# Performance work log

Hardware: AMD Instinct MI355X
Metric: run time of the kernel (lower is better)

Reference implementation:

```python
import jax, jax.numpy as jnp
import numpy as np

OUT_H, OUT_W = 7, 7          # pooled output size
MAX_GRID = 4                 # static bound on adaptive sampling grid (ROI sizes <= 28 px)


def _axis_interp(pos, size, grid_mask):
    """torchvision bilinear rules along one axis.
    pos: sample coords, grid_mask: which adaptive-grid slots are active.
    Returns low/high indices and masked interpolation weights."""
    valid = (pos >= -1.0) & (pos <= size)          # outside -> contributes 0
    p = jnp.maximum(pos, 0.0)
    low = jnp.minimum(jnp.floor(p).astype(jnp.int32), size - 1)
    high = jnp.minimum(low + 1, size - 1)
    p = jnp.where(low >= size - 1, jnp.float32(size - 1), p)  # clamp at top edge
    frac = p - low.astype(p.dtype)
    m = (valid & grid_mask).astype(p.dtype)
    return low, high, (1.0 - frac) * m, frac * m


def _roi_align(features, rois):
    B, C, H, W = features.shape
    bidx = rois[:, 0].astype(jnp.int32)
    x1, y1, x2, y2 = rois[:, 1], rois[:, 2], rois[:, 3], rois[:, 4]
    # spatial_scale = 1.0, aligned=False -> min ROI size of 1
    roi_w = jnp.maximum(x2 - x1, 1.0)
    roi_h = jnp.maximum(y2 - y1, 1.0)
    bin_h = roi_h / OUT_H
    bin_w = roi_w / OUT_W
    # sampling_ratio = -1 -> adaptive grid = ceil(roi_size / pooled_size)
    gh = jnp.clip(jnp.ceil(roi_h / OUT_H).astype(jnp.int32), 1, MAX_GRID)
    gw = jnp.clip(jnp.ceil(roi_w / OUT_W).astype(jnp.int32), 1, MAX_GRID)
    g = jnp.arange(MAX_GRID)
    py = jnp.arange(OUT_H)
    px = jnp.arange(OUT_W)
    # sample coords: [N, OUT, MAX_GRID]
    ys = (y1[:, None, None] + py[None, :, None] * bin_h[:, None, None]
          + (g[None, None, :] + 0.5) * bin_h[:, None, None] / gh[:, None, None].astype(jnp.float32))
    xs = (x1[:, None, None] + px[None, :, None] * bin_w[:, None, None]
          + (g[None, None, :] + 0.5) * bin_w[:, None, None] / gw[:, None, None].astype(jnp.float32))
    gm_y = g[None, None, :] < gh[:, None, None]
    gm_x = g[None, None, :] < gw[:, None, None]
    y_lo, y_hi, wy0, wy1 = _axis_interp(ys, H, gm_y)
    x_lo, x_hi, wx0, wx1 = _axis_interp(xs, W, gm_x)

    f = features.reshape(B, C, H * W)
    bb = bidx[:, None, None, None, None]
    acc = jnp.zeros((rois.shape[0], OUT_H, OUT_W, C), dtype=features.dtype)
    # 4 bilinear corners; gather [N,OH,Gy,OW,Gx,C] one corner at a time
    for yi, wy in ((y_lo, wy0), (y_hi, wy1)):
        for xi, wx in ((x_lo, wx0), (x_hi, wx1)):
            idx = yi[:, :, :, None, None] * W + xi[:, None, None, :, :]  # [N,OH,Gy,OW,Gx]
            vals = f[bb, :, idx]                                         # [N,OH,Gy,OW,Gx,C]
            w = wy[:, :, :, None, None] * wx[:, None, None, :, :]
            acc = acc + jnp.einsum('nygxhc,nygxh->nyxc', vals, w)
    count = jnp.maximum(gh * gw, 1).astype(features.dtype)
    out = acc / count[:, None, None, None]
    return jnp.transpose(out, (0, 3, 1, 2))  # [N, C, OUT_H, OUT_W]


def setup_inputs() -> dict:
    key = jax.random.key(0)
    kf, kb, kx, ky, kw, kh = jax.random.split(key, 6)
    B, C, H, W, N = 4, 256, 200, 272, 512
    features = jax.random.normal(kf, (B, C, H, W), dtype=jnp.float32)
    b = jax.random.randint(kb, (N,), 0, B).astype(jnp.float32)
    # box sizes in [7, 28] px so adaptive grid ceil(size/7) <= MAX_GRID=4
    bw = jax.random.uniform(kw, (N,), minval=7.0, maxval=28.0)
    bh = jax.random.uniform(kh, (N,), minval=7.0, maxval=28.0)
    x1 = jax.random.uniform(kx, (N,), minval=0.0, maxval=W - 29.0)
    y1 = jax.random.uniform(ky, (N,), minval=0.0, maxval=H - 29.0)
    rois = jnp.stack([b, x1, y1, x1 + bw, y1 + bh], axis=1)
    return {"features": features, "rois": rois}


def reference(features, rois):
    return _roi_align(features, rois)
```

## Files before the change

kernel.cpp:

```cpp
#include <hip/hip_runtime.h>

#define MAXG 4
#define CPB 8
#define UCOLS 33
#define PLANE 991
#define S2LEN (4 * PLANE)

__global__ __launch_bounds__(256, 5) void roi_align_kernel(
    const float* __restrict__ feat,
    const float* __restrict__ rois,
    float* __restrict__ out,
    int C, int H, int W)
{
    const int n    = blockIdx.x;
    const int cblk = blockIdx.y;
    const int t    = threadIdx.x;

    __shared__ float2 s_feat2[S2LEN];
    __shared__ int4   s_ypack[28];
    __shared__ int4   s_xpack[28];

    const float* roi = rois + (size_t)n * 5;
    const int   b  = (int)roi[0];
    const float x1 = roi[1], y1 = roi[2], x2 = roi[3], y2 = roi[4];
    const float roi_w = fmaxf(x2 - x1, 1.0f);
    const float roi_h = fmaxf(y2 - y1, 1.0f);
    const float bin_h = roi_h / 7.0f;
    const float bin_w = roi_w / 7.0f;
    int gh = (int)ceilf(roi_h / 7.0f); gh = min(max(gh, 1), MAXG);
    int gw = (int)ceilf(roi_w / 7.0f); gw = min(max(gw, 1), MAXG);
    const float inv_count = 1.0f / (float)(gh * gw);

    auto lo_of = [](float pos, int size) {
        float p = fmaxf(pos, 0.0f);
        return min((int)floorf(p), size - 1);
    };
    const int y0 = lo_of(y1 + 0.5f * bin_h / (float)gh, H);
    const int yE = min(lo_of(y1 + 6.0f * bin_h + ((float)(gh - 1) + 0.5f) * bin_h / (float)gh, H) + 1, H - 1);
    const int x0 = lo_of(x1 + 0.5f * bin_w / (float)gw, W);
    const int xE = min(lo_of(x1 + 6.0f * bin_w + ((float)(gw - 1) + 0.5f) * bin_w / (float)gw, W) + 1, W - 1);
    const int rh    = min(yE - y0 + 1, 30);
    const int x0a   = x0 & ~3;
    const int spanA = min(xE - x0a + 1, 33);
    const int CM    = W - 4 - x0a;

    if (t < 28) {
        const int py = t >> 2, g = t & 3;
        float pos  = y1 + (float)py * bin_h + ((float)g + 0.5f) * bin_h / (float)gh;
        bool valid = (pos >= -1.0f) && (pos <= (float)H);
        float p = fmaxf(pos, 0.0f);
        int lo  = min((int)floorf(p), H - 1);
        int hi  = min(lo + 1, H - 1);
        if (lo >= H - 1) p = (float)(H - 1);
        float frac = p - (float)lo;
        float m = valid ? 1.0f : 0.0f;
        s_ypack[t] = make_int4((lo - y0) * UCOLS, (hi - y0) * UCOLS,
                               __float_as_int((1.0f - frac) * m),
                               __float_as_int(frac * m));
    } else if (t < 56) {
        const int u = t - 28;
        const int px = u >> 2, g = u & 3;
        float pos  = x1 + (float)px * bin_w + ((float)g + 0.5f) * bin_w / (float)gw;
        bool valid = (pos >= -1.0f) && (pos <= (float)W);
        float p = fmaxf(pos, 0.0f);
        int lo  = min((int)floorf(p), W - 1);
        int hi  = min(lo + 1, W - 1);
        if (lo >= W - 1) p = (float)(W - 1);
        float frac = p - (float)lo;
        float m = valid ? 1.0f : 0.0f;
        s_xpack[u] = make_int4(lo - x0a, hi - x0a,
                               __float_as_int((1.0f - frac) * m),
                               __float_as_int(frac * m));
    }

    {
        const int  p    = t & 3;
        const int  q    = (t >> 2) & 7;
        const int  r0   = t >> 5;
        const int  q4   = q << 2;
        const bool qon  = (q4 < spanA);
        const int  colA = min(q4, CM);
        const bool tail = (q == 7) && (spanA == 33);

        const size_t HW = (size_t)H * W;
        const int c0 = cblk * CPB;
        const float* fbase = feat + ((size_t)b * C + c0) * HW + (size_t)y0 * W + x0a;
        const float* ga = fbase + (size_t)(2 * p) * HW;
        float2* sb = s_feat2 + p * PLANE;

        #pragma unroll
        for (int k = 0; k < 4; ++k) {
            const int r = r0 + (k << 3);
            if (r < rh) {
                const float* gp = ga + (size_t)r * W;
                if (qon) {
                    const float4 va = *(const float4*)(gp + colA);
                    const float4 vb = *(const float4*)(gp + HW + colA);
                    float2* sp = sb + r * UCOLS + colA;
                    sp[0] = make_float2(va.x, vb.x);
                    sp[1] = make_float2(va.y, vb.y);
                    sp[2] = make_float2(va.z, vb.z);
                    sp[3] = make_float2(va.w, vb.w);
                }
                if (tail) {
                    sb[r * UCOLS + 32] = make_float2(gp[32], gp[HW + 32]);
                }
            }
        }
    }
    __syncthreads();

    if (t < 196) {
        const int p   = t & 3;
        const int pix = t >> 2;
        const int py  = pix / 7;
        const int px  = pix - py * 7;
        const float2* sp = s_feat2 + p * PLANE;

        int4 xp[4];
        #pragma unroll
        for (int g = 0; g < 4; ++g) xp[g] = s_xpack[(px << 2) + g];

        float ax = 0.0f, ay = 0.0f;
        #pragma unroll
        for (int gy = 0; gy < MAXG; ++gy) {
            if (gy < gh) {
                const int4 yp = s_ypack[(py << 2) + gy];
                const float wy0 = __int_as_float(yp.z);
                const float wy1 = __int_as_float(yp.w);
                #pragma unroll
                for (int gx = 0; gx < MAXG; ++gx) {
                    if (gx < gw) {
                        const float wx0 = __int_as_float(xp[gx].z);
                        const float wx1 = __int_as_float(xp[gx].w);
                        const float2 v00 = sp[yp.x + xp[gx].x];
                        const float2 v01 = sp[yp.x + xp[gx].y];
                        const float2 v10 = sp[yp.y + xp[gx].x];
                        const float2 v11 = sp[yp.y + xp[gx].y];
                        ax += wy0 * (wx0 * v00.x + wx1 * v01.x)
                            + wy1 * (wx0 * v10.x + wx1 * v11.x);
                        ay += wy0 * (wx0 * v00.y + wx1 * v01.y)
                            + wy1 * (wx0 * v10.y + wx1 * v11.y);
                    }
                }
            }
        }
        const size_t ob = ((size_t)n * C + cblk * CPB + 2 * p) * 49 + pix;
        out[ob]      = ax * inv_count;
        out[ob + 49] = ay * inv_count;
    }
}

extern "C" void kernel_launch(void* const* d_in, const int* in_sizes, int n_in,
                              void* d_out, int out_size, void* d_ws, size_t ws_size,
                              hipStream_t stream) {
    const float* feat = (const float*)d_in[0];
    const float* rois = (const float*)d_in[1];
    float* out = (float*)d_out;

    const int C = 256, H = 200, W = 272;
    const int N = in_sizes[1] / 5;

    dim3 grid(N, C / CPB);
    roi_align_kernel<<<grid, 256, 0, stream>>>(feat, rois, out, C, H, W);
}
```

Before: 323.8 us.

## Process four ROIs per block with register-prefetched feature loads overlapping compute

Each block now handles four consecutive ROIs instead of one. While the current ROI's outputs are computed from shared memory, the next ROI's feature patch is loaded from global memory into registers, then written to shared memory after a barrier. The aim is to hide global load latency behind the interpolation math and to spread per-block launch overhead across more work. The cost is more registers (launch bounds lowered from 5 to 4 waves), extra barriers, and a grid that is four times smaller.

```diff
diff --git a/kernel.cpp b/kernel.cpp
--- a/kernel.cpp
+++ b/kernel.cpp
@@ -5,112 +5,134 @@
 #define UCOLS 33
 #define PLANE 991
 #define S2LEN (4 * PLANE)
-
-__global__ __launch_bounds__(256, 5) void roi_align_kernel(
-    const float* __restrict__ feat,
-    const float* __restrict__ rois,
-    float* __restrict__ out,
-    int C, int H, int W)
-{
-    const int n    = blockIdx.x;
-    const int cblk = blockIdx.y;
-    const int t    = threadIdx.x;
-
-    __shared__ float2 s_feat2[S2LEN];
-    __shared__ int4   s_ypack[28];
-    __shared__ int4   s_xpack[28];
-
+#define RPB 4
+
+
+struct RoiS {
+    float x1, y1, bin_h, bin_w;
+    int   gh, gw;
+    float inv_count;
+    int   y0, x0a, rh, spanA, CM;
+    const float* fbase;
+};
+
+__device__ __forceinline__ int lo_of(float pos, int size) {
+    float pp = fmaxf(pos, 0.0f);
+    return min((int)floorf(pp), size - 1);
+}
+
+__device__ __forceinline__ RoiS make_scalars(const float* __restrict__ rois, int n,
+                                             const float* __restrict__ feat,
+                                             int C, int c0, int H, int W, size_t HW) {
+    RoiS s;
     const float* roi = rois + (size_t)n * 5;
     const int   b  = (int)roi[0];
     const float x1 = roi[1], y1 = roi[2], x2 = roi[3], y2 = roi[4];
     const float roi_w = fmaxf(x2 - x1, 1.0f);
     const float roi_h = fmaxf(y2 - y1, 1.0f);
-    const float bin_h = roi_h / 7.0f;
-    const float bin_w = roi_w / 7.0f;
+    s.bin_h = roi_h / 7.0f;
+    s.bin_w = roi_w / 7.0f;
     int gh = (int)ceilf(roi_h / 7.0f); gh = min(max(gh, 1), MAXG);
     int gw = (int)ceilf(roi_w / 7.0f); gw = min(max(gw, 1), MAXG);
-    const float inv_count = 1.0f / (float)(gh * gw);
-
-    auto lo_of = [](float pos, int size) {
-        float p = fmaxf(pos, 0.0f);
-        return min((int)floorf(p), size - 1);
-    };
-    const int y0 = lo_of(y1 + 0.5f * bin_h / (float)gh, H);
-    const int yE = min(lo_of(y1 + 6.0f * bin_h + ((float)(gh - 1) + 0.5f) * bin_h / (float)gh, H) + 1, H - 1);
-    const int x0 = lo_of(x1 + 0.5f * bin_w / (float)gw, W);
-    const int xE = min(lo_of(x1 + 6.0f * bin_w + ((float)(gw - 1) + 0.5f) * bin_w / (float)gw, W) + 1, W - 1);
-    const int rh    = min(yE - y0 + 1, 30);
-    const int x0a   = x0 & ~3;
-    const int spanA = min(xE - x0a + 1, 33);
-    const int CM    = W - 4 - x0a;
-
+    s.gh = gh; s.gw = gw;
+    s.inv_count = 1.0f / (float)(gh * gw);
+    s.x1 = x1; s.y1 = y1;
+    s.y0 = lo_of(y1 + 0.5f * s.bin_h / (float)gh, H);
+    int yE = min(lo_of(y1 + 6.0f * s.bin_h + ((float)(gh - 1) + 0.5f) * s.bin_h / (float)gh, H) + 1, H - 1);
+    int x0 = lo_of(x1 + 0.5f * s.bin_w / (float)gw, W);
+    int xE = min(lo_of(x1 + 6.0f * s.bin_w + ((float)(gw - 1) + 0.5f) * s.bin_w / (float)gw, W) + 1, W - 1);
+    s.rh    = min(yE - s.y0 + 1, 30);
+    s.x0a   = x0 & ~3;
+    s.spanA = min(xE - s.x0a + 1, 33);
+    s.CM    = W - 4 - s.x0a;
+    s.fbase = feat + ((size_t)b * C + c0) * HW + (size_t)s.y0 * W + s.x0a;
+    return s;
+}
+
+__device__ __forceinline__ void issue_loads(const RoiS& s, int p, int q, int q4, int r0,
+                                            size_t HW, int W,
+                                            float4 va[4], float4 vb[4], float tc[4][2]) {
+    const bool qon  = (q4 < s.spanA);
+    const int  colA = min(q4, s.CM);
+    const bool tail = (q == 7) && (s.spanA == 33);
+    const float* ga = s.fbase + (size_t)(2 * p) * HW;
+    #pragma unroll
+    for (int k = 0; k < 4; ++k) {
+        const int r = r0 + (k << 3);
+        if (r < s.rh) {
+            const float* gp = ga + (size_t)r * W;
+            if (qon) {
+                va[k] = *(const float4*)(gp + colA);
+                vb[k] = *(const float4*)(gp + HW + colA);
+            }
+            if (tail) { tc[k][0] = gp[32]; tc[k][1] = gp[HW + 32]; }
+        }
+    }
+}
+
+__device__ __forceinline__ void write_lds(const RoiS& s, int p, int q, int q4, int r0,
+                                          float2* __restrict__ s_feat2,
+                                          const float4 va[4], const float4 vb[4],
+                                          const float tc[4][2]) {
+    const bool qon  = (q4 < s.spanA);
+    const int  colA = min(q4, s.CM);
+    const bool tail = (q == 7) && (s.spanA == 33);
+    float2* sb = s_feat2 + p * PLANE;
+    #pragma unroll
+    for (int k = 0; k < 4; ++k) {
+        const int r = r0 + (k << 3);
+        if (r < s.rh) {
+            if (qon) {
+                float2* sp = sb + r * UCOLS + colA;
+                sp[0] = make_float2(va[k].x, vb[k].x);
+                sp[1] = make_float2(va[k].y, vb[k].y);
+                sp[2] = make_float2(va[k].z, vb[k].z);
+                sp[3] = make_float2(va[k].w, vb[k].w);
+            }
+            if (tail) sb[r * UCOLS + 32] = make_float2(tc[k][0], tc[k][1]);
+        }
+    }
+}
+
+__device__ __forceinline__ void write_tables(const RoiS& s, int t, int H, int W,
+                                             int4* __restrict__ s_ypack,
+                                             int4* __restrict__ s_xpack) {
     if (t < 28) {
         const int py = t >> 2, g = t & 3;
-        float pos  = y1 + (float)py * bin_h + ((float)g + 0.5f) * bin_h / (float)gh;
+        float pos  = s.y1 + (float)py * s.bin_h + ((float)g + 0.5f) * s.bin_h / (float)s.gh;
         bool valid = (pos >= -1.0f) && (pos <= (float)H);
-        float p = fmaxf(pos, 0.0f);
-        int lo  = min((int)floorf(p), H - 1);
+        float pp = fmaxf(pos, 0.0f);
+        int lo  = min((int)floorf(pp), H - 1);
         int hi  = min(lo + 1, H - 1);
-        if (lo >= H - 1) p = (float)(H - 1);
-        float frac = p - (float)lo;
+        if (lo >= H - 1) pp = (float)(H - 1);
+        float frac = pp - (float)lo;
         float m = valid ? 1.0f : 0.0f;
-        s_ypack[t] = make_int4((lo - y0) * UCOLS, (hi - y0) * UCOLS,
+        s_ypack[t] = make_int4((lo - s.y0) * UCOLS, (hi - s.y0) * UCOLS,
                                __float_as_int((1.0f - frac) * m),
                                __float_as_int(frac * m));
     } else if (t < 56) {
         const int u = t - 28;
         const int px = u >> 2, g = u & 3;
-        float pos  = x1 + (float)px * bin_w + ((float)g + 0.5f) * bin_w / (float)gw;
+        float pos  = s.x1 + (float)px * s.bin_w + ((float)g + 0.5f) * s.bin_w / (float)s.gw;
         bool valid = (pos >= -1.0f) && (pos <= (float)W);
-        float p = fmaxf(pos, 0.0f);
-        int lo  = min((int)floorf(p), W - 1);
+        float pp = fmaxf(pos, 0.0f);
+        int lo  = min((int)floorf(pp), W - 1);
         int hi  = min(lo + 1, W - 1);
-        if (lo >= W - 1) p = (float)(W - 1);
-        float frac = p - (float)lo;
+        if (lo >= W - 1) pp = (float)(W - 1);
+        float frac = pp - (float)lo;
         float m = valid ? 1.0f : 0.0f;
-        s_xpack[u] = make_int4(lo - x0a, hi - x0a,
+        s_xpack[u] = make_int4(lo - s.x0a, hi - s.x0a,
                                __float_as_int((1.0f - frac) * m),
                                __float_as_int(frac * m));
     }
-
-    {
-        const int  p    = t & 3;
-        const int  q    = (t >> 2) & 7;
-        const int  r0   = t >> 5;
-        const int  q4   = q << 2;
-        const bool qon  = (q4 < spanA);
-        const int  colA = min(q4, CM);
-        const bool tail = (q == 7) && (spanA == 33);
-
-        const size_t HW = (size_t)H * W;
-        const int c0 = cblk * CPB;
-        const float* fbase = feat + ((size_t)b * C + c0) * HW + (size_t)y0 * W + x0a;
-        const float* ga = fbase + (size_t)(2 * p) * HW;
-        float2* sb = s_feat2 + p * PLANE;
-
-        #pragma unroll
-        for (int k = 0; k < 4; ++k) {
-            const int r = r0 + (k << 3);
-            if (r < rh) {
-                const float* gp = ga + (size_t)r * W;
-                if (qon) {
-                    const float4 va = *(const float4*)(gp + colA);
-                    const float4 vb = *(const float4*)(gp + HW + colA);
-                    float2* sp = sb + r * UCOLS + colA;
-                    sp[0] = make_float2(va.x, vb.x);
-                    sp[1] = make_float2(va.y, vb.y);
-                    sp[2] = make_float2(va.z, vb.z);
-                    sp[3] = make_float2(va.w, vb.w);
-                }
-                if (tail) {
-                    sb[r * UCOLS + 32] = make_float2(gp[32], gp[HW + 32]);
-                }
-            }
-        }
-    }
-    __syncthreads();
-
-    if (t < 196) {
+}
+
+__device__ __forceinline__ void compute_out(const RoiS& s, int n, int cblk, int t, bool nvalid,
+                                            const float2* __restrict__ s_feat2,
+                                            const int4* __restrict__ s_ypack,
+                                            const int4* __restrict__ s_xpack,
+                                            float* __restrict__ out, int C) {
+    if (t < 196 && nvalid) {
         const int p   = t & 3;
         const int pix = t >> 2;
         const int py  = pix / 7;
@@ -124,13 +146,13 @@
         float ax = 0.0f, ay = 0.0f;
         #pragma unroll
         for (int gy = 0; gy < MAXG; ++gy) {
-            if (gy < gh) {
+            if (gy < s.gh) {
                 const int4 yp = s_ypack[(py << 2) + gy];
                 const float wy0 = __int_as_float(yp.z);
                 const float wy1 = __int_as_float(yp.w);
                 #pragma unroll
                 for (int gx = 0; gx < MAXG; ++gx) {
-                    if (gx < gw) {
+                    if (gx < s.gw) {
                         const float wx0 = __int_as_float(xp[gx].z);
                         const float wx1 = __int_as_float(xp[gx].w);
                         const float2 v00 = sp[yp.x + xp[gx].x];
@@ -146,8 +168,58 @@
             }
         }
         const size_t ob = ((size_t)n * C + cblk * CPB + 2 * p) * 49 + pix;
-        out[ob]      = ax * inv_count;
-        out[ob + 49] = ay * inv_count;
+        out[ob]      = ax * s.inv_count;
+        out[ob + 49] = ay * s.inv_count;
+    }
+}
+
+__global__ __launch_bounds__(256, 4) void roi_align_kernel(
+    const float* __restrict__ feat,
+    const float* __restrict__ rois,
+    float* __restrict__ out,
+    int C, int H, int W, int N)
+{
+    const int n0   = blockIdx.x * RPB;
+    const int cblk = blockIdx.y;
+    const int t    = threadIdx.x;
+
+    __shared__ float2 s_feat2[S2LEN];
+    __shared__ int4   s_ypack[28];
+    __shared__ int4   s_xpack[28];
+
+    const size_t HW = (size_t)H * W;
+    const int c0 = cblk * CPB;
+
+    const int p  = t & 3;
+    const int q  = (t >> 2) & 7;
+    const int r0 = t >> 5;
+    const int q4 = q << 2;
+
+    float4 va[4], vb[4];
+    float  tc[4][2];
+
+    RoiS cur = make_scalars(rois, min(n0, N - 1), feat, C, c0, H, W, HW);
+    issue_loads(cur, p, q, q4, r0, HW, W, va, vb, tc);
+    write_tables(cur, t, H, W, s_ypack, s_xpack);
+    write_lds(cur, p, q, q4, r0, s_feat2, va, vb, tc);
+    __syncthreads();
+
+    #pragma unroll
+    for (int i = 0; i < RPB; ++i) {
+        RoiS nxt;
+        if (i + 1 < RPB) {
+            nxt = make_scalars(rois, min(n0 + i + 1, N - 1), feat, C, c0, H, W, HW);
+            issue_loads(nxt, p, q, q4, r0, HW, W, va, vb, tc);
+        }
+        compute_out(cur, n0 + i, cblk, t, (n0 + i) < N,
+                    s_feat2, s_ypack, s_xpack, out, C);
+        if (i + 1 < RPB) {
+            __syncthreads();
+            write_tables(nxt, t, H, W, s_ypack, s_xpack);
+            write_lds(nxt, p, q, q4, r0, s_feat2, va, vb, tc);
+            __syncthreads();
+            cur = nxt;
+        }
     }
 }
 
@@ -161,6 +233,6 @@
     const int C = 256, H = 200, W = 272;
     const int N = in_sizes[1] / 5;
 
-    dim3 grid(N, C / CPB);
-    roi_align_kernel<<<grid, 256, 0, stream>>>(feat, rois, out, C, H, W);
-}
+    dim3 grid((N + RPB - 1) / RPB, C / CPB);
+    roi_align_kernel<<<grid, 256, 0, stream>>>(feat, rois, out, C, H, W, N);
+}
```

Measured after the change: 335.7 us. +3.7%, slower.

## Sort ROIs by Morton order and remap workgroups so each XCD handles nearby ROIs

Applied to the files above, without the earlier changes.

Adds a single-block bitonic sort that orders ROIs by a Morton code of their quantized centers and writes the permutation to workspace. The main kernel switches to a 1D grid whose workgroup index is decoded so that each of the 8 XCDs gets a contiguous chunk of 64 spatially sorted ROIs across all channel blocks. The goal is for overlapping ROIs to reuse feature lines in each XCD's L2 instead of fetching them repeatedly from HBM. The cost is an extra serial kernel launch. The layout also hardcodes N<=512 and assumes round-robin dispatch of workgroups across XCDs.

```diff
diff --git a/kernel.cpp b/kernel.cpp
--- a/kernel.cpp
+++ b/kernel.cpp
@@ -5,16 +5,64 @@
 #define UCOLS 33
 #define PLANE 991
 #define S2LEN (4 * PLANE)
+#define NXCD 8
+#define CHUNK 64
+
+
+__global__ void roi_sort_kernel(const float* __restrict__ rois,
+                                int* __restrict__ perm, int N) {
+    __shared__ unsigned int sk[512];
+    const int t = threadIdx.x;
+    for (int i = t; i < 512; i += 256) {
+        unsigned int key = 0xFFFFFFFFu;
+        if (i < N) {
+            const float* r = rois + (size_t)i * 5;
+            float yc = r[2] + r[4];
+            float xc = r[1] + r[3];
+            unsigned int yq = (unsigned int)min(max((int)(yc * 0.625f),  0), 255);
+            unsigned int xq = (unsigned int)min(max((int)(xc * 0.4697f), 0), 255);
+            unsigned int x = xq, y = yq;
+            x = (x | (x << 4)) & 0x0F0Fu; x = (x | (x << 2)) & 0x3333u; x = (x | (x << 1)) & 0x5555u;
+            y = (y | (y << 4)) & 0x0F0Fu; y = (y | (y << 2)) & 0x3333u; y = (y | (y << 1)) & 0x5555u;
+            unsigned int mort = (y << 1) | x;
+            key = (mort << 9) | (unsigned int)i;
+        }
+        sk[i] = key;
+    }
+    __syncthreads();
+    for (int k = 2; k <= 512; k <<= 1) {
+        for (int j = k >> 1; j > 0; j >>= 1) {
+            for (int i = t; i < 512; i += 256) {
+                const int ixj = i ^ j;
+                if (ixj > i) {
+                    unsigned int a = sk[i], b = sk[ixj];
+                    const bool up = ((i & k) == 0);
+                    if (up ? (a > b) : (a < b)) { sk[i] = b; sk[ixj] = a; }
+                }
+            }
+            __syncthreads();
+        }
+    }
+    for (int i = t; i < 512; i += 256)
+        if (i < N) perm[i] = (int)(sk[i] & 511u);
+}
 
 __global__ __launch_bounds__(256, 5) void roi_align_kernel(
     const float* __restrict__ feat,
     const float* __restrict__ rois,
+    const int* __restrict__ perm,
     float* __restrict__ out,
-    int C, int H, int W)
+    int C, int H, int W, int N)
 {
-    const int n    = blockIdx.x;
-    const int cblk = blockIdx.y;
-    const int t    = threadIdx.x;
+    const int wg   = blockIdx.x;
+    const int xcd  = wg & (NXCD - 1);
+    const int sfl  = wg >> 3;
+    const int slot = sfl & (CHUNK - 1);
+    const int cblk = sfl >> 6;
+    const int nidx = (xcd << 6) + slot;
+    if (nidx >= N) return;
+    const int n = perm[nidx];
+    const int t = threadIdx.x;
 
     __shared__ float2 s_feat2[S2LEN];
     __shared__ int4   s_ypack[28];
@@ -157,10 +205,13 @@
     const float* feat = (const float*)d_in[0];
     const float* rois = (const float*)d_in[1];
     float* out = (float*)d_out;
+    int* perm = (int*)d_ws;
 
     const int C = 256, H = 200, W = 272;
     const int N = in_sizes[1] / 5;
 
-    dim3 grid(N, C / CPB);
-    roi_align_kernel<<<grid, 256, 0, stream>>>(feat, rois, out, C, H, W);
+    roi_sort_kernel<<<1, 256, 0, stream>>>(rois, perm, N);
+
+    dim3 grid(NXCD * CHUNK * (C / CPB));
+    roi_align_kernel<<<grid, 256, 0, stream>>>(feat, rois, perm, out, C, H, W, N);
 }
```

Measured after the change: 342.9 us. 5.9% more time.
